# Kernel tuning notes

Measured on AMD Instinct MI355X. Metric: run time of the kernel, lower is better.

Reference implementation:

```python
import jax, jax.numpy as jnp
from jax import lax
import numpy as np

KS, STRIDE, RATE, SCALE = 3, 1, 2, 10.0  # module init kwargs


def _resize_bilinear_ac(x, oh, ow):
    # F.interpolate(mode='bilinear', align_corners=True); x: [B,C,H,W]
    H, W = x.shape[2], x.shape[3]
    ys = jnp.linspace(0.0, H - 1.0, oh)
    xs = jnp.linspace(0.0, W - 1.0, ow)
    y0 = jnp.floor(ys).astype(jnp.int32)
    y1 = jnp.minimum(y0 + 1, H - 1)
    wy = (ys - y0)[:, None]
    x0 = jnp.floor(xs).astype(jnp.int32)
    x1 = jnp.minimum(x0 + 1, W - 1)
    wx = xs - x0
    g = lambda yi, xi: x[:, :, yi, :][:, :, :, xi]
    top = g(y0, x0) * (1 - wx) + g(y0, x1) * wx
    bot = g(y1, x0) * (1 - wx) + g(y1, x1) * wx
    return top * (1 - wy) + bot * wy


def _conv3x3(x, w, b):
    y = lax.conv_general_dilated(x, w, (1, 1), ((1, 1), (1, 1)),
                                 dimension_numbers=('NCHW', 'OIHW', 'NCHW'))
    return y + b[None, :, None, None]


def _extract_patches(x, k, s):
    # mirrors extract_patches(): ZeroPad2d(1) when k != 1, then unfold h,w
    if k != 1:
        x = jnp.pad(x, ((0, 0), (0, 0), (1, 1), (1, 1)))
    b, c, h, w = x.shape
    nh = (h - k) // s + 1
    nw = (w - k) // s + 1
    cols = jnp.stack([x[:, :, i:i + s * (nh - 1) + 1:s, j:j + s * (nw - 1) + 1:s]
                      for i in range(k) for j in range(k)], axis=-1)  # [B,C,nh,nw,k*k]
    return cols.reshape(b, c, nh, nw, k, k).transpose(0, 2, 3, 1, 4, 5).reshape(b, nh * nw, c, k, k)


def _instance_norm(x, eps=1e-5):
    mu = x.mean((2, 3), keepdims=True)
    var = ((x - mu) ** 2).mean((2, 3), keepdims=True)
    return (x - mu) * lax.rsqrt(var + eps)


def _conv_transpose(att, w):
    # torch F.conv_transpose2d(att, w, stride=2, padding=1); att [Q,h,w], w [Q,Cout,4,4]
    rhs = jnp.flip(w, (-2, -1)).transpose(1, 0, 2, 3)  # [Cout,Q,4,4]
    return lax.conv_general_dilated(att[None], rhs, (1, 1), ((2, 2), (2, 2)),
                                    lhs_dilation=(2, 2),
                                    dimension_numbers=('NCHW', 'OIHW', 'NCHW'))[0]


def _forward(background, foreground, mask, Wc, bc, Wm, bm, Wf, bf):
    h, w = foreground.shape[2], foreground.shape[3]
    mask64 = _resize_bilinear_ac(mask, h, w)
    fg_c = foreground * (1 - mask64)
    fg_m = foreground * mask64
    bg_c = background * (1 - mask64)
    bg_m = background * mask64
    # ODConv2d(fg, bg) stand-in: plain 3x3 conv on the fused features
    bg_c = _conv3x3(fg_c + bg_c, Wc, bc)
    bg_m = _conv3x3(fg_m + bg_m, Wm, bm)
    x = _conv3x3(bg_c + bg_m, Wf, bf)
    x = _instance_norm(x)
    x = x * jax.nn.sigmoid(x)  # MemoryEfficientSwish
    b = x.shape[0]
    raw_w = _extract_patches(x, 2 * RATE, STRIDE * RATE)       # [B,1024,256,4,4]
    x_down = _resize_bilinear_ac(x, h // RATE, w // RATE)       # [B,256,32,32]
    hd, wd = x_down.shape[2], x_down.shape[3]
    pt = _extract_patches(x_down, KS, STRIDE)                   # [B,1024,256,3,3]
    mask32 = _resize_bilinear_ac(mask64, hd, wd)
    mpt = _extract_patches(mask32, KS, STRIDE)                  # [B,1024,1,3,3]
    mm = (mpt.mean((2, 3, 4)) == 0.0).astype(x.dtype)[:, :, None, None]  # [B,1024,1,1]
    norm = jnp.sqrt((pt * pt).sum((2, 3, 4), keepdims=True))
    w_normed = pt / jnp.maximum(norm, 1e-4)
    # score = F.conv2d(x_down, w_normed, padding=1): batched patch-attention GEMM
    score = jnp.einsum('bqckl,bpckl->bqp', w_normed, pt).reshape(b, hd * wd, hd, wd)
    score = score * mm
    att = jax.nn.softmax(score * SCALE, axis=1) * mm
    att = jnp.clip(att, 1e-8, None)
    f1 = jax.vmap(_conv_transpose)(att, raw_w) / 4.0            # [B,256,64,64]
    return f1 * mask64 + x * (1 - mask64)


def setup_inputs() -> dict:
    key = jax.random.key(0)
    ks = jax.random.split(key, 9)
    B, C, H, W = 8, 256, 64, 64
    background = jax.random.normal(ks[0], (B, C, H, W), jnp.float32)
    foreground = jax.random.normal(ks[1], (B, C, H, W), jnp.float32)
    # blocky binary hole mask (16x16 blocks upsampled to 256x256)
    m0 = (jax.random.uniform(ks[2], (B, 1, 16, 16)) > 0.5).astype(jnp.float32)
    mask = jnp.repeat(jnp.repeat(m0, 16, axis=2), 16, axis=3)
    s = 0.05
    Wc = jax.random.normal(ks[3], (256, 256, 3, 3), jnp.float32) * s
    bc = jax.random.normal(ks[4], (256,), jnp.float32) * s
    Wm = jax.random.normal(ks[5], (256, 256, 3, 3), jnp.float32) * s
    bm = jax.random.normal(ks[6], (256,), jnp.float32) * s
    Wf = jax.random.normal(ks[7], (256, 256, 3, 3), jnp.float32) * s
    bf = jax.random.normal(ks[8], (256,), jnp.float32) * s
    return {'background': background, 'foreground': foreground, 'mask': mask,
            'Wc': Wc, 'bc': bc, 'Wm': Wm, 'bm': bm, 'Wf': Wf, 'bf': bf}


def reference(background, foreground, mask, Wc, bc, Wm, bm, Wf, bf):
    return _forward(background, foreground, mask, Wc, bc, Wm, bm, Wf, bf)
```

## Files before the change

kernel.cpp:

```cpp
#include <hip/hip_runtime.h>
#include <math.h>

#define B_ 8
#define C_ 256
#define NPIX 4096
#define NP 1024

typedef __attribute__((ext_vector_type(8))) short bf16x8;
typedef __attribute__((ext_vector_type(4))) float f32x4;

#define GLL16(src, dst) __builtin_amdgcn_global_load_lds( \
    (__attribute__((address_space(1))) void*)(src), \
    (__attribute__((address_space(3))) void*)(dst), 16, 0, 0)

__device__ __forceinline__ unsigned short f2bf(float f) {
  unsigned int u = __float_as_uint(f);
  unsigned int r = (u + 0x7FFFu + ((u >> 16) & 1u)) >> 16;
  return (unsigned short)r;
}
__device__ __forceinline__ unsigned int pk2(unsigned short lo, unsigned short hi) {
  return (unsigned int)lo | ((unsigned int)hi << 16);
}

__device__ __forceinline__ float wave_reduce_sum(float v) {
#pragma unroll
  for (int off = 32; off > 0; off >>= 1) v += __shfl_down(v, off, 64);
  return v;
}
__device__ __forceinline__ float wave_reduce_max(float v) {
#pragma unroll
  for (int off = 32; off > 0; off >>= 1) v = fmaxf(v, __shfl_down(v, off, 64));
  return v;
}

__global__ __launch_bounds__(256) void k_resize(const float* __restrict__ in, float* __restrict__ out,
                                                int IH, int IW, int OH, int OW, int nElem) {
  int idx = blockIdx.x * 256 + threadIdx.x;
  if (idx >= nElem) return;
  int ox = idx % OW; int t = idx / OW; int oy = t % OH; int bc = t / OH;
  float dy = (float)(IH - 1) / (float)(OH - 1);
  float dx = (float)(IW - 1) / (float)(OW - 1);
  float yf = (float)oy * dy;
  float xf = (float)ox * dx;
  float y0f = floorf(yf), x0f = floorf(xf);
  int y0 = (int)y0f, x0 = (int)x0f;
  int y1 = min(y0 + 1, IH - 1), x1 = min(x0 + 1, IW - 1);
  float wy = yf - y0f, wx = xf - x0f;
  const float* p = in + (size_t)bc * IH * IW;
  float a = p[y0 * IW + x0], b = p[y0 * IW + x1];
  float c = p[y1 * IW + x0], d = p[y1 * IW + x1];
  float top = a * (1.0f - wx) + b * wx;
  float bot = c * (1.0f - wx) + d * wx;
  out[idx] = top * (1.0f - wy) + bot * wy;
}

__global__ __launch_bounds__(256) void k_wprep(const float* __restrict__ Wc, const float* __restrict__ Wm,
                                               const float* __restrict__ Wf,
                                               unsigned short* __restrict__ Wp1, unsigned short* __restrict__ Wp2) {
  int idx = blockIdx.x * 256 + threadIdx.x;
  if (idx >= 3 * 589824) return;
  int part = idx / 589824;
  int rem = idx % 589824;
  int kk = rem >> 16, co = (rem >> 8) & 255, ci = rem & 255;
  const float* W = (part == 0) ? Wc : (part == 1) ? Wm : Wf;
  unsigned short o = f2bf(W[(size_t)co * 2304 + ci * 9 + kk]);
  if (part == 0) Wp1[rem] = o;
  else if (part == 1) Wp1[589824 + rem] = o;
  else Wp2[rem] = o;
}

__global__ __launch_bounds__(256) void k_bias(const float* __restrict__ bc, const float* __restrict__ bm,
                                              float* __restrict__ bias1, float* __restrict__ zpg) {
  int i = threadIdx.x;
  bias1[i] = bc[i] + bm[i];
  for (int j = i; j < 2048; j += 256) zpg[j] = 0.f;
}

__global__ __launch_bounds__(256) void k_prepAT(const float* __restrict__ fg, const float* __restrict__ bg,
                                                const float* __restrict__ m64,
                                                unsigned short* __restrict__ A0t, unsigned short* __restrict__ A1t) {
  __shared__ unsigned short T0[64][66];
  __shared__ unsigned short T1[64][66];
  int pt = blockIdx.x, ct = blockIdx.y, b = blockIdx.z;
  int pix0 = pt << 6, ci0 = ct << 6;
  int tid = threadIdx.x;
  {
    int r = tid >> 2, c4 = (tid & 3) << 4;
    size_t ib = (((size_t)(b * 256 + ci0 + r)) << 12) + pix0 + c4;
    const float* fb = fg + ib;
    const float* gb = bg + ib;
    const float* mb = m64 + (((size_t)b) << 12) + pix0 + c4;
#pragma unroll
    for (int k = 0; k < 16; k += 4) {
      float4 f = *(const float4*)(fb + k);
      float4 g = *(const float4*)(gb + k);
      float4 m = *(const float4*)(mb + k);
      float s0 = f.x + g.x, s1 = f.y + g.y, s2 = f.z + g.z, s3 = f.w + g.w;
      T0[r][c4 + k + 0] = f2bf(s0 * (1.f - m.x));
      T0[r][c4 + k + 1] = f2bf(s1 * (1.f - m.y));
      T0[r][c4 + k + 2] = f2bf(s2 * (1.f - m.z));
      T0[r][c4 + k + 3] = f2bf(s3 * (1.f - m.w));
      T1[r][c4 + k + 0] = f2bf(s0 * m.x);
      T1[r][c4 + k + 1] = f2bf(s1 * m.y);
      T1[r][c4 + k + 2] = f2bf(s2 * m.z);
      T1[r][c4 + k + 3] = f2bf(s3 * m.w);
    }
  }
  __syncthreads();
  {
    int pr = tid >> 2, cc = (tid & 3) << 4;
    unsigned int o0[8], o1[8];
#pragma unroll
    for (int k = 0; k < 8; k++) {
      o0[k] = pk2(T0[cc + 2 * k][pr], T0[cc + 2 * k + 1][pr]);
      o1[k] = pk2(T1[cc + 2 * k][pr], T1[cc + 2 * k + 1][pr]);
    }
    size_t ob = ((((size_t)b << 12) + pix0 + pr) << 8) + ci0 + cc;
    *(uint4*)&A0t[ob] = *(uint4*)&o0[0];
    *(uint4*)&A0t[ob + 8] = *(uint4*)&o0[4];
    *(uint4*)&A1t[ob] = *(uint4*)&o1[0];
    *(uint4*)&A1t[ob + 8] = *(uint4*)&o1[4];
  }
}

__device__ __forceinline__ int swz(int row, int slot) {
  return row * 32 + ((slot ^ (row & 3) ^ ((row >> 2) & 3)) << 3);
}

template <int NKK, bool OUT_TRANS_BF16>
__global__ __launch_bounds__(256, 2) void k_conv2ph(const unsigned short* __restrict__ A0t,
                                                    const unsigned short* __restrict__ A1t,
                                                    const unsigned short* __restrict__ Wp,
                                                    const float* __restrict__ bias,
                                                    const unsigned short* __restrict__ zp,
                                                    void* __restrict__ outp) {
  __shared__ __align__(16) unsigned short AB[2][8192];
  int wgl = blockIdx.x + 32 * (blockIdx.y + 2 * blockIdx.z);
  int nid = (wgl & 7) * 64 + (wgl >> 3);
  int bp = nid & 31, cot = (nid >> 5) & 1, b = nid >> 6;
  int tid = threadIdx.x, lane = tid & 63, w3 = tid >> 6;
  int wm = w3 >> 1, wn = w3 & 1;

  int rA = w3 * 32 + (lane >> 2), rA1 = rA + 16;
  int ds0 = (lane & 3) ^ (rA & 3) ^ ((rA >> 2) & 3);
  int ds1 = (lane & 3) ^ (rA1 & 3) ^ ((rA1 >> 2) & 3);
  int y_0 = bp * 2 + (rA >> 6), x_0 = rA & 63;
  int y_1 = bp * 2 + (rA1 >> 6), x_1 = rA1 & 63;
  int co_0 = cot * 128 + rA, co_1 = cot * 128 + rA1;

  f32x4 acc[4][4];
#pragma unroll
  for (int i = 0; i < 4; i++)
#pragma unroll
    for (int j = 0; j < 4; j++) acc[i][j] = (f32x4){0.f, 0.f, 0.f, 0.f};

  const unsigned short *pA0, *pA1, *pB0, *pB1;

#define UPDATE(kkv) {                                                           \
    int kk_ = (kkv);                                                            \
    int kw_ = (NKK == 18 && kk_ >= 9) ? kk_ - 9 : kk_;                          \
    const unsigned short* Asrc_ = (NKK == 18 && kk_ >= 9) ? A1t : A0t;          \
    int ky_ = kw_ / 3 - 1, kx_ = kw_ % 3 - 1;                                   \
    int yy0_ = y_0 + ky_, xx0_ = x_0 + kx_;                                     \
    int yy1_ = y_1 + ky_, xx1_ = x_1 + kx_;                                     \
    pA0 = ((unsigned)yy0_ < 64u && (unsigned)xx0_ < 64u)                        \
        ? Asrc_ + ((((size_t)(b << 6) + yy0_) << 6) + xx0_) * 256 + ds0 * 8     \
        : zp + ds0 * 8;                                                         \
    pA1 = ((unsigned)yy1_ < 64u && (unsigned)xx1_ < 64u)                        \
        ? Asrc_ + ((((size_t)(b << 6) + yy1_) << 6) + xx1_) * 256 + ds1 * 8     \
        : zp + ds1 * 8;                                                         \
    pB0 = Wp + ((size_t)kk_ << 16) + co_0 * 256 + ds0 * 8;                      \
    pB1 = Wp + ((size_t)kk_ << 16) + co_1 * 256 + ds1 * 8;                      \
  }
#define STAGE(c2, buf) {                                                        \
    int ci0_ = ((c2) & 7) << 5;                                                 \
    unsigned short* lb_ = &AB[buf][0];                                          \
    GLL16(pA0 + ci0_, lb_ + w3 * 1024);                                         \
    GLL16(pA1 + ci0_, lb_ + w3 * 1024 + 512);                                   \
    GLL16(pB0 + ci0_, lb_ + 4096 + w3 * 1024);                                  \
    GLL16(pB1 + ci0_, lb_ + 4096 + w3 * 1024 + 512);                            \
  }

  const int NCH = NKK * 8;
  UPDATE(0);
  STAGE(0, 0);
  for (int c = 0; c < NCH; ++c) {
    asm volatile("" ::: "memory");
    __builtin_amdgcn_s_barrier();
    asm volatile("" ::: "memory");
    if (c < NCH - 1) {
      int cn = c + 1;
      if ((cn & 7) == 0) UPDATE(cn >> 3);
      STAGE(cn, cn & 1);
      asm volatile("s_waitcnt vmcnt(4)" ::: "memory");
    } else {
      asm volatile("s_waitcnt vmcnt(0)" ::: "memory");
    }
    __builtin_amdgcn_s_barrier();
    asm volatile("" ::: "memory");
    const unsigned short* Al = &AB[c & 1][0];
    const unsigned short* Bl = &AB[c & 1][4096];
    int slot = lane >> 4;
    int mr = wm * 64 + (lane & 15), ncc = wn * 64 + (lane & 15);
    bf16x8 af[4], bfr[4];
#pragma unroll
    for (int i = 0; i < 4; i++) af[i] = *(const bf16x8*)&Al[swz(mr + i * 16, slot)];
#pragma unroll
    for (int j = 0; j < 4; j++) bfr[j] = *(const bf16x8*)&Bl[swz(ncc + j * 16, slot)];
#pragma unroll
    for (int i = 0; i < 4; i++)
#pragma unroll
      for (int j = 0; j < 4; j++)
        acc[i][j] = __builtin_amdgcn_mfma_f32_16x16x32_bf16(af[i], bfr[j], acc[i][j], 0, 0, 0);
  }
#undef STAGE
#undef UPDATE

  int px0 = bp * 128 + wm * 64 + ((lane >> 4) << 2);
  int co0 = cot * 128 + wn * 64 + (lane & 15);
#pragma unroll
  for (int j = 0; j < 4; j++) {
    int co = co0 + j * 16;
    float bs = bias[co];
#pragma unroll
    for (int i = 0; i < 4; i++) {
#pragma unroll
      for (int r = 0; r < 4; r++) {
        float v = acc[i][j][r] + bs;
        int pix = px0 + i * 16 + r;
        if (OUT_TRANS_BF16)
          ((unsigned short*)outp)[((((size_t)b << 12) + pix) << 8) + co] = f2bf(v);
        else
          ((float*)outp)[((((size_t)b << 8) + co) << 12) + pix] = v;
      }
    }
  }
}

__global__ __launch_bounds__(256) void k_innorm(float* __restrict__ x) {
  __shared__ float s4[4];
  int bc = blockIdx.x;
  float* p = x + (size_t)bc * NPIX;
  int tid = threadIdx.x;
  int lane = tid & 63, w = tid >> 6;
  float v[16];
  float s = 0.f;
#pragma unroll
  for (int i = 0; i < 16; i++) { v[i] = p[tid + i * 256]; s += v[i]; }
  s = wave_reduce_sum(s);
  if (lane == 0) s4[w] = s;
  __syncthreads();
  float mean = (s4[0] + s4[1] + s4[2] + s4[3]) * (1.0f / 4096.0f);
  __syncthreads();
  float s2 = 0.f;
#pragma unroll
  for (int i = 0; i < 16; i++) { float d = v[i] - mean; s2 += d * d; }
  s2 = wave_reduce_sum(s2);
  if (lane == 0) s4[w] = s2;
  __syncthreads();
  float var = (s4[0] + s4[1] + s4[2] + s4[3]) * (1.0f / 4096.0f);
  float inv = 1.0f / sqrtf(var + 1e-5f);
#pragma unroll
  for (int i = 0; i < 16; i++) {
    float xn = (v[i] - mean) * inv;
    float sg = 1.0f / (1.0f + expf(-xn));
    p[tid + i * 256] = xn * sg;
  }
}

__global__ __launch_bounds__(256) void k_trans_xd(const float* __restrict__ xd,
                                                  unsigned short* __restrict__ xdt) {
  __shared__ unsigned short T[64][66];
  int qt = blockIdx.x, ct = blockIdx.y, b = blockIdx.z;
  int q0 = qt << 6, ci0 = ct << 6;
  int tid = threadIdx.x;
  {
    int r = tid >> 2, c4 = (tid & 3) << 4;
    const float* xb = xd + (((size_t)(b * 256 + ci0 + r)) << 10) + q0 + c4;
#pragma unroll
    for (int k = 0; k < 16; k += 4) {
      float4 f = *(const float4*)(xb + k);
      T[r][c4 + k + 0] = f2bf(f.x);
      T[r][c4 + k + 1] = f2bf(f.y);
      T[r][c4 + k + 2] = f2bf(f.z);
      T[r][c4 + k + 3] = f2bf(f.w);
    }
  }
  __syncthreads();
  {
    int qr = tid >> 2, cc = (tid & 3) << 4;
    unsigned int o[8];
#pragma unroll
    for (int k = 0; k < 8; k++) o[k] = pk2(T[cc + 2 * k][qr], T[cc + 2 * k + 1][qr]);
    size_t ob = ((((size_t)b << 10) + q0 + qr) << 8) + ci0 + cc;
    *(uint4*)&xdt[ob] = *(uint4*)&o[0];
    *(uint4*)&xdt[ob + 8] = *(uint4*)&o[4];
  }
}

__global__ __launch_bounds__(256) void k_sq32(const float* __restrict__ xd, float* __restrict__ sq) {
  int idx = blockIdx.x * 256 + threadIdx.x;
  if (idx >= B_ * NP) return;
  int pix = idx & 1023; int b = idx >> 10;
  const float* p = xd + (size_t)b * C_ * NP + pix;
  float s = 0.f;
  for (int c = 0; c < C_; c++) { float v = p[c * NP]; s += v * v; }
  sq[idx] = s;
}

__global__ __launch_bounds__(256) void k_normmm(const float* __restrict__ sq, const float* __restrict__ m32,
                                                float* __restrict__ fq) {
  int idx = blockIdx.x * 256 + threadIdx.x;
  if (idx >= B_ * NP) return;
  int q = idx & 1023, b = idx >> 10;
  int qi = q >> 5, qj = q & 31;
  float ns = 0.f, ms = 0.f;
#pragma unroll
  for (int k = 0; k < 3; k++)
#pragma unroll
    for (int l = 0; l < 3; l++) {
      int r = qi + k - 1, c = qj + l - 1;
      if (r >= 0 && r < 32 && c >= 0 && c < 32) {
        ns += sq[b * NP + r * 32 + c];
        ms += m32[b * NP + r * 32 + c];
      }
    }
  float f = (ms == 0.0f) ? (1.0f / fmaxf(sqrtf(ns), 1e-4f)) : 0.0f;
  fq[idx] = f;
}

__global__ __launch_bounds__(256, 2) void k_gram2ph(const unsigned short* __restrict__ xdt,
                                                    const float* __restrict__ fq,
                                                    const unsigned short* __restrict__ zp,
                                                    float* __restrict__ sc) {
  __shared__ __align__(16) unsigned short AB[2][8192];
  int wgl = blockIdx.x + 8 * (blockIdx.y + 8 * blockIdx.z);
  int nid = (wgl & 7) * 64 + (wgl >> 3);
  int bp = nid & 7, bq = (nid >> 3) & 7, b = nid >> 6;
  int tid = threadIdx.x, lane = tid & 63, w3 = tid >> 6;
  int wm = w3 >> 1, wn = w3 & 1;

  int rA = w3 * 32 + (lane >> 2), rA1 = rA + 16;
  int ds0 = (lane & 3) ^ (rA & 3) ^ ((rA >> 2) & 3);
  int ds1 = (lane & 3) ^ (rA1 & 3) ^ ((rA1 >> 2) & 3);
  int pA0r = bp * 128 + rA, pA1r = bp * 128 + rA1;
  int pB0r = bq * 128 + rA, pB1r = bq * 128 + rA1;
  int piA0 = pA0r >> 5, pjA0 = pA0r & 31, piA1 = pA1r >> 5, pjA1 = pA1r & 31;
  int piB0 = pB0r >> 5, pjB0 = pB0r & 31, piB1 = pB1r >> 5, pjB1 = pB1r & 31;
  const unsigned short* xb = xdt + (((size_t)b) << 18);

  f32x4 acc[4][4];
#pragma unroll
  for (int i = 0; i < 4; i++)
#pragma unroll
    for (int j = 0; j < 4; j++) acc[i][j] = (f32x4){0.f, 0.f, 0.f, 0.f};

  const unsigned short *pA0, *pA1, *pB0, *pB1;

#define GUPDATE(kkv) {                                                          \
    int kk_ = (kkv);                                                            \
    int dy_ = kk_ / 3 - 1, dx_ = kk_ % 3 - 1;                                   \
    int ya0 = piA0 + dy_, xa0 = pjA0 + dx_;                                     \
    int ya1 = piA1 + dy_, xa1 = pjA1 + dx_;                                     \
    int yb0 = piB0 + dy_, xb0 = pjB0 + dx_;                                     \
    int yb1 = piB1 + dy_, xb1 = pjB1 + dx_;                                     \
    pA0 = ((unsigned)ya0 < 32u && (unsigned)xa0 < 32u)                          \
        ? xb + ((((size_t)ya0 << 5) + xa0) << 8) + ds0 * 8 : zp + ds0 * 8;      \
    pA1 = ((unsigned)ya1 < 32u && (unsigned)xa1 < 32u)                          \
        ? xb + ((((size_t)ya1 << 5) + xa1) << 8) + ds1 * 8 : zp + ds1 * 8;      \
    pB0 = ((unsigned)yb0 < 32u && (unsigned)xb0 < 32u)                          \
        ? xb + ((((size_t)yb0 << 5) + xb0) << 8) + ds0 * 8 : zp + ds0 * 8;      \
    pB1 = ((unsigned)yb1 < 32u && (unsigned)xb1 < 32u)                          \
        ? xb + ((((size_t)yb1 << 5) + xb1) << 8) + ds1 * 8 : zp + ds1 * 8;      \
  }
#define GSTAGE(c2, buf) {                                                       \
    int ci0_ = ((c2) & 7) << 5;                                                 \
    unsigned short* lb_ = &AB[buf][0];                                          \
    GLL16(pA0 + ci0_, lb_ + w3 * 1024);                                         \
    GLL16(pA1 + ci0_, lb_ + w3 * 1024 + 512);                                   \
    GLL16(pB0 + ci0_, lb_ + 4096 + w3 * 1024);                                  \
    GLL16(pB1 + ci0_, lb_ + 4096 + w3 * 1024 + 512);                            \
  }

  GUPDATE(0);
  GSTAGE(0, 0);
  for (int c = 0; c < 72; ++c) {
    asm volatile("" ::: "memory");
    __builtin_amdgcn_s_barrier();
    asm volatile("" ::: "memory");
    if (c < 71) {
      int cn = c + 1;
      if ((cn & 7) == 0) GUPDATE(cn >> 3);
      GSTAGE(cn, cn & 1);
      asm volatile("s_waitcnt vmcnt(4)" ::: "memory");
    } else {
      asm volatile("s_waitcnt vmcnt(0)" ::: "memory");
    }
    __builtin_amdgcn_s_barrier();
    asm volatile("" ::: "memory");
    const unsigned short* Al = &AB[c & 1][0];
    const unsigned short* Bl = &AB[c & 1][4096];
    int slot = lane >> 4;
    int mr = wm * 64 + (lane & 15), ncc = wn * 64 + (lane & 15);
    bf16x8 af[4], bfr[4];
#pragma unroll
    for (int i = 0; i < 4; i++) af[i] = *(const bf16x8*)&Al[swz(mr + i * 16, slot)];
#pragma unroll
    for (int j = 0; j < 4; j++) bfr[j] = *(const bf16x8*)&Bl[swz(ncc + j * 16, slot)];
#pragma unroll
    for (int i = 0; i < 4; i++)
#pragma unroll
      for (int j = 0; j < 4; j++)
        acc[i][j] = __builtin_amdgcn_mfma_f32_16x16x32_bf16(af[i], bfr[j], acc[i][j], 0, 0, 0);
  }
#undef GSTAGE
#undef GUPDATE

  int q0 = bq * 128 + wn * 64 + (lane & 15);
  int p0 = bp * 128 + wm * 64 + ((lane >> 4) << 2);
#pragma unroll
  for (int j = 0; j < 4; j++) {
    int q = q0 + j * 16;
    float f = fq[(b << 10) + q];
#pragma unroll
    for (int i = 0; i < 4; i++)
#pragma unroll
      for (int r = 0; r < 4; r++)
        sc[((size_t)(b << 10) + (p0 + i * 16 + r)) * NP + q] = acc[i][j][r] * f;
  }
}

__global__ __launch_bounds__(256) void k_softmax(const float* __restrict__ sc, const float* __restrict__ fq,
                                                 unsigned short* __restrict__ attb) {
  __shared__ float s4[4];
  int row = blockIdx.x;
  int b = row >> 10;
  const float* r = sc + (size_t)row * NP;
  int tid = threadIdx.x;
  int lane = tid & 63, w = tid >> 6;
  float4 sv = *(const float4*)&r[tid * 4];
  float l0 = sv.x * 10.f, l1 = sv.y * 10.f, l2 = sv.z * 10.f, l3 = sv.w * 10.f;
  float mx = fmaxf(fmaxf(l0, l1), fmaxf(l2, l3));
  mx = wave_reduce_max(mx);
  if (lane == 0) s4[w] = mx;
  __syncthreads();
  float M = fmaxf(fmaxf(s4[0], s4[1]), fmaxf(s4[2], s4[3]));
  __syncthreads();
  float e0 = expf(l0 - M), e1 = expf(l1 - M), e2 = expf(l2 - M), e3 = expf(l3 - M);
  float s = e0 + e1 + e2 + e3;
  s = wave_reduce_sum(s);
  if (lane == 0) s4[w] = s;
  __syncthreads();
  float inv = 1.0f / (s4[0] + s4[1] + s4[2] + s4[3]);
  const float* fb = fq + b * NP + tid * 4;
  float m0 = fb[0] > 0.f ? 1.f : 0.f;
  float m1 = fb[1] > 0.f ? 1.f : 0.f;
  float m2 = fb[2] > 0.f ? 1.f : 0.f;
  float m3 = fb[3] > 0.f ? 1.f : 0.f;
  float a0 = fmaxf(e0 * inv * m0, 1e-8f);
  float a1 = fmaxf(e1 * inv * m1, 1e-8f);
  float a2 = fmaxf(e2 * inv * m2, 1e-8f);
  float a3 = fmaxf(e3 * inv * m3, 1e-8f);
  uint2 o;
  o.x = pk2(f2bf(a0), f2bf(a1));
  o.y = pk2(f2bf(a2), f2bf(a3));
  *(uint2*)&attb[(size_t)row * NP + tid * 4] = o;
}

__global__ __launch_bounds__(256) void k_xprep(const float* __restrict__ x,
                                               unsigned short* __restrict__ P0,
                                               unsigned short* __restrict__ P1,
                                               unsigned short* __restrict__ P2) {
  int idx = blockIdx.x * 256 + threadIdx.x;
  int xh8 = idx & 3;
  int yh = (idx >> 2) & 31;
  int co = (idx >> 7) & 255;
  int pc = (idx >> 15) & 3;
  int b  = idx >> 17;
  int cy = pc >> 1, cx = pc & 1;
  const float* row = x + ((size_t)(b * 256 + co) * 64 + (2 * yh + cy)) * 64 + 16 * xh8;
  float4 f0 = *(const float4*)(row);
  float4 f1 = *(const float4*)(row + 4);
  float4 f2 = *(const float4*)(row + 8);
  float4 f3 = *(const float4*)(row + 12);
  unsigned short v0 = f2bf(cx ? f0.y : f0.x), v1 = f2bf(cx ? f0.w : f0.z);
  unsigned short v2 = f2bf(cx ? f1.y : f1.x), v3 = f2bf(cx ? f1.w : f1.z);
  unsigned short v4 = f2bf(cx ? f2.y : f2.x), v5 = f2bf(cx ? f2.w : f2.z);
  unsigned short v6 = f2bf(cx ? f3.y : f3.x), v7 = f2bf(cx ? f3.w : f3.z);
  int prev = __shfl_up((int)v7, 1, 64);
  int next = __shfl_down((int)v0, 1, 64);
  unsigned short pv = (xh8 == 0) ? (unsigned short)0 : (unsigned short)prev;
  unsigned short nx = (xh8 == 3) ? (unsigned short)0 : (unsigned short)next;
  size_t base = ((size_t)((b * 4 + pc) * 256 + co) * 32 + yh) * 32 + 8 * xh8;
  uint4 w0 = {pk2(v0, v1), pk2(v2, v3), pk2(v4, v5), pk2(v6, v7)};
  *(uint4*)&P0[base] = w0;
  uint4 w1 = {pk2(pv, v0), pk2(v1, v2), pk2(v3, v4), pk2(v5, v6)};
  *(uint4*)&P1[base] = w1;
  uint4 w2 = {pk2(v1, v2), pk2(v3, v4), pk2(v5, v6), pk2(v7, nx)};
  *(uint4*)&P2[base] = w2;
}

__global__ __launch_bounds__(256, 2) void k_pv(const unsigned short* __restrict__ attb,
                                               const unsigned short* __restrict__ P0,
                                               const unsigned short* __restrict__ P1,
                                               const unsigned short* __restrict__ P2,
                                               const unsigned short* __restrict__ zp,
                                               const float* __restrict__ xbuf,
                                               const float* __restrict__ m64,
                                               float* __restrict__ out) {
  __shared__ __align__(16) unsigned short AB[2][8192];
  int wg = blockIdx.x + blockIdx.y * 8 + blockIdx.z * 16;
  int nid = (wg & 7) * 64 + (wg >> 3);
  int bn = nid & 7, bm = (nid >> 3) & 1, z = nid >> 4;
  int b = z >> 2, cls = z & 3, cy = cls >> 1, cx = cls & 1;
  int tid = threadIdx.x, lane = tid & 63, w3 = tid >> 6;
  int wm = w3 >> 1, wn = w3 & 1;

  int dy1 = cy ? -1 : 1;
  int pio1 = cy ? 1 : -1;
  int pjo1 = cx ? 1 : -1;
  const unsigned short* Pdx = cx ? P1 : P2;

  int rA0 = w3 * 32 + (lane >> 2);
  int rA1 = rA0 + 16;
  int ds0 = (lane & 3) ^ (rA0 & 3) ^ ((rA0 >> 2) & 3);
  int ds1 = (lane & 3) ^ (rA1 & 3) ^ ((rA1 >> 2) & 3);
  int offA0 = ((z * 256 + bm * 128 + rA0) << 10) + ds0 * 8;
  int offA1 = ((z * 256 + bm * 128 + rA1) << 10) + ds1 * 8;

  const unsigned short* attB = attb + ((size_t)b << 20);
  int o0 = bn * 128 + rA0, o1 = bn * 128 + rA1;
  int oy0 = o0 >> 5, ox0 = o0 & 31, oy1 = o1 >> 5, ox1 = o1 & 31;
#define BPTR(oyv, oxv, dsv, tyv, txv) ({                                        \
    int pi = (oyv) + ((tyv) ? pio1 : 0);                                        \
    int pj = (oxv) + ((txv) ? pjo1 : 0);                                        \
    (pi >= 0 && pi < 32 && pj >= 0 && pj < 32)                                  \
        ? attB + (((pi << 5) + pj) << 10) + (dsv) * 8 : zp; })
  const unsigned short* b0t0 = BPTR(oy0, ox0, ds0, 0, 0);
  const unsigned short* b0t1 = BPTR(oy0, ox0, ds0, 0, 1);
  const unsigned short* b0t2 = BPTR(oy0, ox0, ds0, 1, 0);
  const unsigned short* b0t3 = BPTR(oy0, ox0, ds0, 1, 1);
  const unsigned short* b1t0 = BPTR(oy1, ox1, ds1, 0, 0);
  const unsigned short* b1t1 = BPTR(oy1, ox1, ds1, 0, 1);
  const unsigned short* b1t2 = BPTR(oy1, ox1, ds1, 1, 0);
  const unsigned short* b1t3 = BPTR(oy1, ox1, ds1, 1, 1);
#undef BPTR

  f32x4 acc[4][4];
#pragma unroll
  for (int i = 0; i < 4; i++)
#pragma unroll
    for (int j = 0; j < 4; j++) acc[i][j] = (f32x4){0.f, 0.f, 0.f, 0.f};

  int dA0 = w3 * 1024, dA1 = w3 * 1024 + 512;
  int dB0 = 4096 + w3 * 1024, dB1 = 4096 + w3 * 1024 + 512;

#define PSTAGE(c2, buf) {                                                       \
    int t2 = (c2) >> 5, qi = (c2) & 31;                                         \
    int q32 = qi * 32;                                                          \
    const unsigned short* Ab = (t2 & 1) ? Pdx : P0;                             \
    int dyo = (t2 >> 1) ? dy1 * 32 : 0;                                         \
    bool vA = (t2 < 2) || ((dy1 > 0) ? (qi < 31) : (qi > 0));                   \
    if (!vA) Ab = zp;                                                           \
    int oA0 = vA ? offA0 + dyo + q32 : 0;                                       \
    int oA1 = vA ? offA1 + dyo + q32 : 0;                                       \
    unsigned short* lb = &AB[buf][0];                                           \
    GLL16(Ab + oA0, lb + dA0);                                                  \
    GLL16(Ab + oA1, lb + dA1);                                                  \
    const unsigned short* sB0 = (t2 == 0 ? b0t0 : t2 == 1 ? b0t1 : t2 == 2 ? b0t2 : b0t3) + q32; \
    const unsigned short* sB1 = (t2 == 0 ? b1t0 : t2 == 1 ? b1t1 : t2 == 2 ? b1t2 : b1t3) + q32; \
    GLL16(sB0, lb + dB0);                                                       \
    GLL16(sB1, lb + dB1);                                                       \
  }

  PSTAGE(0, 0);
  for (int c = 0; c < 128; ++c) {
    asm volatile("" ::: "memory");
    __builtin_amdgcn_s_barrier();
    asm volatile("" ::: "memory");
    if (c < 127) {
      PSTAGE(c + 1, (c + 1) & 1);
      asm volatile("s_waitcnt vmcnt(4)" ::: "memory");
    } else {
      asm volatile("s_waitcnt vmcnt(0)" ::: "memory");
    }
    __builtin_amdgcn_s_barrier();
    asm volatile("" ::: "memory");
    const unsigned short* Al = &AB[c & 1][0];
    const unsigned short* Bl = &AB[c & 1][4096];
    int slot = lane >> 4;
    int mr = wm * 64 + (lane & 15), ncc = wn * 64 + (lane & 15);
    bf16x8 af[4], bfr[4];
#pragma unroll
    for (int i = 0; i < 4; i++) af[i] = *(const bf16x8*)&Al[swz(mr + i * 16, slot)];
#pragma unroll
    for (int j = 0; j < 4; j++) bfr[j] = *(const bf16x8*)&Bl[swz(ncc + j * 16, slot)];
#pragma unroll
    for (int i = 0; i < 4; i++)
#pragma unroll
      for (int j = 0; j < 4; j++)
        acc[i][j] = __builtin_amdgcn_mfma_f32_16x16x32_bf16(af[i], bfr[j], acc[i][j], 0, 0, 0);
  }
#undef PSTAGE

  int co0 = bm * 128 + wm * 64 + ((lane >> 4) << 2);
  int oo0 = bn * 128 + wn * 64 + (lane & 15);
#pragma unroll
  for (int j = 0; j < 4; j++) {
    int o = oo0 + j * 16;
    int oy = ((o >> 5) << 1) + cy, ox = ((o & 31) << 1) + cx;
    int opix = oy * 64 + ox;
    float msk = m64[b * NPIX + opix];
    float s = 0.25f * msk, t1m = 1.0f - msk;
#pragma unroll
    for (int i = 0; i < 4; i++) {
#pragma unroll
      for (int r = 0; r < 4; r++) {
        int co = co0 + i * 16 + r;
        size_t xi = (size_t)(b * C_ + co) * NPIX + opix;
        out[xi] = acc[i][j][r] * s + xbuf[xi] * t1m;
      }
    }
  }
}

extern "C" void kernel_launch(void* const* d_in, const int* in_sizes, int n_in,
                              void* d_out, int out_size, void* d_ws, size_t ws_size,
                              hipStream_t stream) {
  const float* bg   = (const float*)d_in[0];
  const float* fg   = (const float*)d_in[1];
  const float* mask = (const float*)d_in[2];
  const float* Wc   = (const float*)d_in[3];
  const float* bc   = (const float*)d_in[4];
  const float* Wm   = (const float*)d_in[5];
  const float* bm   = (const float*)d_in[6];
  const float* Wf   = (const float*)d_in[7];
  const float* bf   = (const float*)d_in[8];
  float* out = (float*)d_out;
  float* w = (float*)d_ws;

  float* mask64 = w;
  float* mask32 = w + 32768;
  float* sq32   = w + 40960;
  float* fq     = w + 49152;
  float* bias1  = w + 57344;
  float* zpage  = w + 57600;
  unsigned short* A0t = (unsigned short*)(w + 65536);
  unsigned short* A1t = (unsigned short*)(w + 65536 + 4194304);
  float* sc = w + 65536;
  unsigned short* P0u = (unsigned short*)(w + 65536);
  unsigned short* P1u = (unsigned short*)(w + 4259840);
  unsigned short* tbuf_t = (unsigned short*)(w + 8454144);
  float* xd = w + 8454144;
  unsigned short* xdt = (unsigned short*)(w + 10551296);
  unsigned short* attb = (unsigned short*)(w + 8454144);
  float* xbuf = w + 12648448;
  unsigned short* Wp1 = (unsigned short*)(w + 21037056);
  unsigned short* Wp2 = (unsigned short*)(w + 21626880);
  unsigned short* P2u = (unsigned short*)(w + 21037056);

  const unsigned short* zp = (const unsigned short*)zpage;

  hipLaunchKernelGGL(k_resize, dim3(128), dim3(256), 0, stream, mask, mask64, 256, 256, 64, 64, 32768);
  hipLaunchKernelGGL(k_wprep, dim3(6912), dim3(256), 0, stream, Wc, Wm, Wf, Wp1, Wp2);
  hipLaunchKernelGGL(k_bias, dim3(1), dim3(256), 0, stream, bc, bm, bias1, zpage);
  hipLaunchKernelGGL(k_prepAT, dim3(64, 4, 8), dim3(256), 0, stream, fg, bg, mask64, A0t, A1t);
  hipLaunchKernelGGL((k_conv2ph<18, true>), dim3(32, 2, 8), dim3(256), 0, stream,
                     A0t, A1t, Wp1, bias1, zp, (void*)tbuf_t);
  hipLaunchKernelGGL((k_conv2ph<9, false>), dim3(32, 2, 8), dim3(256), 0, stream,
                     tbuf_t, tbuf_t, Wp2, bf, zp, (void*)xbuf);
  hipLaunchKernelGGL(k_innorm, dim3(B_ * C_), dim3(256), 0, stream, xbuf);
  hipLaunchKernelGGL(k_resize, dim3(8192), dim3(256), 0, stream, xbuf, xd, 64, 64, 32, 32, B_ * C_ * NP);
  hipLaunchKernelGGL(k_resize, dim3(32), dim3(256), 0, stream, mask64, mask32, 64, 64, 32, 32, B_ * NP);
  hipLaunchKernelGGL(k_trans_xd, dim3(16, 4, 8), dim3(256), 0, stream, xd, xdt);
  hipLaunchKernelGGL(k_sq32, dim3(32), dim3(256), 0, stream, xd, sq32);
  hipLaunchKernelGGL(k_normmm, dim3(32), dim3(256), 0, stream, sq32, mask32, fq);
  hipLaunchKernelGGL(k_gram2ph, dim3(8, 8, 8), dim3(256), 0, stream, xdt, fq, zp, sc);
  hipLaunchKernelGGL(k_softmax, dim3(B_ * NP), dim3(256), 0, stream, sc, fq, attb);
  hipLaunchKernelGGL(k_xprep, dim3(4096), dim3(256), 0, stream, xbuf, P0u, P1u, P2u);
  hipLaunchKernelGGL(k_pv, dim3(8, 2, 32), dim3(256), 0, stream, attb, P0u, P1u, P2u,
                     zp, xbuf, mask64, out);
}
```

Baseline: 356.1 us.

## Double K-chunk per barrier in MFMA GEMMs and fuse norm with downsample

```diff
diff --git a/kernel.cpp b/kernel.cpp
--- a/kernel.cpp
+++ b/kernel.cpp
@@ -134,7 +134,7 @@
                                                     const float* __restrict__ bias,
                                                     const unsigned short* __restrict__ zp,
                                                     void* __restrict__ outp) {
-  __shared__ __align__(16) unsigned short AB[2][8192];
+  __shared__ __align__(16) unsigned short AB[2][16384];
   int wgl = blockIdx.x + 32 * (blockIdx.y + 2 * blockIdx.z);
   int nid = (wgl & 7) * 64 + (wgl >> 3);
   int bp = nid & 31, cot = (nid >> 5) & 1, b = nid >> 6;
@@ -173,15 +173,19 @@
     pB1 = Wp + ((size_t)kk_ << 16) + co_1 * 256 + ds1 * 8;                      \
   }
 #define STAGE(c2, buf) {                                                        \
-    int ci0_ = ((c2) & 7) << 5;                                                 \
+    int ci0_ = ((c2) & 3) << 6;                                                 \
     unsigned short* lb_ = &AB[buf][0];                                          \
-    GLL16(pA0 + ci0_, lb_ + w3 * 1024);                                         \
-    GLL16(pA1 + ci0_, lb_ + w3 * 1024 + 512);                                   \
-    GLL16(pB0 + ci0_, lb_ + 4096 + w3 * 1024);                                  \
-    GLL16(pB1 + ci0_, lb_ + 4096 + w3 * 1024 + 512);                            \
-  }
-
-  const int NCH = NKK * 8;
+    GLL16(pA0 + ci0_,      lb_ + w3 * 1024);                                    \
+    GLL16(pA1 + ci0_,      lb_ + w3 * 1024 + 512);                              \
+    GLL16(pA0 + ci0_ + 32, lb_ + 4096 + w3 * 1024);                             \
+    GLL16(pA1 + ci0_ + 32, lb_ + 4096 + w3 * 1024 + 512);                       \
+    GLL16(pB0 + ci0_,      lb_ + 8192 + w3 * 1024);                             \
+    GLL16(pB1 + ci0_,      lb_ + 8192 + w3 * 1024 + 512);                       \
+    GLL16(pB0 + ci0_ + 32, lb_ + 12288 + w3 * 1024);                            \
+    GLL16(pB1 + ci0_ + 32, lb_ + 12288 + w3 * 1024 + 512);                      \
+  }
+
+  const int NCH = NKK * 4;
   UPDATE(0);
   STAGE(0, 0);
   for (int c = 0; c < NCH; ++c) {
@@ -190,28 +194,31 @@
     asm volatile("" ::: "memory");
     if (c < NCH - 1) {
       int cn = c + 1;
-      if ((cn & 7) == 0) UPDATE(cn >> 3);
+      if ((cn & 3) == 0) UPDATE(cn >> 2);
       STAGE(cn, cn & 1);
-      asm volatile("s_waitcnt vmcnt(4)" ::: "memory");
+      asm volatile("s_waitcnt vmcnt(8)" ::: "memory");
     } else {
       asm volatile("s_waitcnt vmcnt(0)" ::: "memory");
     }
     __builtin_amdgcn_s_barrier();
     asm volatile("" ::: "memory");
-    const unsigned short* Al = &AB[c & 1][0];
-    const unsigned short* Bl = &AB[c & 1][4096];
     int slot = lane >> 4;
     int mr = wm * 64 + (lane & 15), ncc = wn * 64 + (lane & 15);
-    bf16x8 af[4], bfr[4];
-#pragma unroll
-    for (int i = 0; i < 4; i++) af[i] = *(const bf16x8*)&Al[swz(mr + i * 16, slot)];
-#pragma unroll
-    for (int j = 0; j < 4; j++) bfr[j] = *(const bf16x8*)&Bl[swz(ncc + j * 16, slot)];
-#pragma unroll
-    for (int i = 0; i < 4; i++)
-#pragma unroll
-      for (int j = 0; j < 4; j++)
-        acc[i][j] = __builtin_amdgcn_mfma_f32_16x16x32_bf16(af[i], bfr[j], acc[i][j], 0, 0, 0);
+#pragma unroll
+    for (int ks = 0; ks < 2; ++ks) {
+      const unsigned short* Al = &AB[c & 1][ks << 12];
+      const unsigned short* Bl = &AB[c & 1][8192 + (ks << 12)];
+      bf16x8 af[4], bfr[4];
+#pragma unroll
+      for (int i = 0; i < 4; i++) af[i] = *(const bf16x8*)&Al[swz(mr + i * 16, slot)];
+#pragma unroll
+      for (int j = 0; j < 4; j++) bfr[j] = *(const bf16x8*)&Bl[swz(ncc + j * 16, slot)];
+#pragma unroll
+      for (int i = 0; i < 4; i++)
+#pragma unroll
+        for (int j = 0; j < 4; j++)
+          acc[i][j] = __builtin_amdgcn_mfma_f32_16x16x32_bf16(af[i], bfr[j], acc[i][j], 0, 0, 0);
+    }
   }
 #undef STAGE
 #undef UPDATE
@@ -237,7 +244,8 @@
   }
 }
 
-__global__ __launch_bounds__(256) void k_innorm(float* __restrict__ x) {
+__global__ __launch_bounds__(256) void k_post(float* __restrict__ x, float* __restrict__ xd) {
+  __shared__ float sL[4096];
   __shared__ float s4[4];
   int bc = blockIdx.x;
   float* p = x + (size_t)bc * NPIX;
@@ -264,7 +272,28 @@
   for (int i = 0; i < 16; i++) {
     float xn = (v[i] - mean) * inv;
     float sg = 1.0f / (1.0f + expf(-xn));
-    p[tid + i * 256] = xn * sg;
+    float o = xn * sg;
+    p[tid + i * 256] = o;
+    sL[tid + i * 256] = o;
+  }
+  __syncthreads();
+  float dyx = 63.0f / 31.0f;
+  float* xdp = xd + (size_t)bc * NP;
+#pragma unroll
+  for (int k = 0; k < 4; k++) {
+    int q = tid + k * 256;
+    int yq = q >> 5, xq = q & 31;
+    float yf = (float)yq * dyx;
+    float xf = (float)xq * dyx;
+    float y0f = floorf(yf), x0f = floorf(xf);
+    int y0 = (int)y0f, x0 = (int)x0f;
+    int y1 = min(y0 + 1, 63), x1 = min(x0 + 1, 63);
+    float wy = yf - y0f, wx = xf - x0f;
+    float a = sL[y0 * 64 + x0], b2 = sL[y0 * 64 + x1];
+    float c2 = sL[y1 * 64 + x0], d2 = sL[y1 * 64 + x1];
+    float top = a * (1.0f - wx) + b2 * wx;
+    float bot = c2 * (1.0f - wx) + d2 * wx;
+    xdp[q] = top * (1.0f - wy) + bot * wy;
   }
 }
 
@@ -308,12 +337,14 @@
   sq[idx] = s;
 }
 
-__global__ __launch_bounds__(256) void k_normmm(const float* __restrict__ sq, const float* __restrict__ m32,
-                                                float* __restrict__ fq) {
+__global__ __launch_bounds__(256) void k_fq(const float* __restrict__ sq, const float* __restrict__ m64,
+                                            float* __restrict__ fq) {
   int idx = blockIdx.x * 256 + threadIdx.x;
   if (idx >= B_ * NP) return;
   int q = idx & 1023, b = idx >> 10;
   int qi = q >> 5, qj = q & 31;
+  const float* mb = m64 + (b << 12);
+  float dyx = 63.0f / 31.0f;
   float ns = 0.f, ms = 0.f;
 #pragma unroll
   for (int k = 0; k < 3; k++)
@@ -322,7 +353,16 @@
       int r = qi + k - 1, c = qj + l - 1;
       if (r >= 0 && r < 32 && c >= 0 && c < 32) {
         ns += sq[b * NP + r * 32 + c];
-        ms += m32[b * NP + r * 32 + c];
+        float yf = (float)r * dyx, xf = (float)c * dyx;
+        float y0f = floorf(yf), x0f = floorf(xf);
+        int y0 = (int)y0f, x0 = (int)x0f;
+        int y1 = min(y0 + 1, 63), x1 = min(x0 + 1, 63);
+        float wy = yf - y0f, wx = xf - x0f;
+        float a = mb[y0 * 64 + x0], b2 = mb[y0 * 64 + x1];
+        float c2 = mb[y1 * 64 + x0], d2 = mb[y1 * 64 + x1];
+        float top = a * (1.0f - wx) + b2 * wx;
+        float bot = c2 * (1.0f - wx) + d2 * wx;
+        ms += top * (1.0f - wy) + bot * wy;
       }
     }
   float f = (ms == 0.0f) ? (1.0f / fmaxf(sqrtf(ns), 1e-4f)) : 0.0f;
@@ -333,7 +373,7 @@
                                                     const float* __restrict__ fq,
                                                     const unsigned short* __restrict__ zp,
                                                     float* __restrict__ sc) {
-  __shared__ __align__(16) unsigned short AB[2][8192];
+  __shared__ __align__(16) unsigned short AB[2][16384];
   int wgl = blockIdx.x + 8 * (blockIdx.y + 8 * blockIdx.z);
   int nid = (wgl & 7) * 64 + (wgl >> 3);
   int bp = nid & 7, bq = (nid >> 3) & 7, b = nid >> 6;
@@ -374,44 +414,51 @@
         ? xb + ((((size_t)yb1 << 5) + xb1) << 8) + ds1 * 8 : zp + ds1 * 8;      \
   }
 #define GSTAGE(c2, buf) {                                                       \
-    int ci0_ = ((c2) & 7) << 5;                                                 \
+    int ci0_ = ((c2) & 3) << 6;                                                 \
     unsigned short* lb_ = &AB[buf][0];                                          \
-    GLL16(pA0 + ci0_, lb_ + w3 * 1024);                                         \
-    GLL16(pA1 + ci0_, lb_ + w3 * 1024 + 512);                                   \
-    GLL16(pB0 + ci0_, lb_ + 4096 + w3 * 1024);                                  \
-    GLL16(pB1 + ci0_, lb_ + 4096 + w3 * 1024 + 512);                            \
+    GLL16(pA0 + ci0_,      lb_ + w3 * 1024);                                    \
+    GLL16(pA1 + ci0_,      lb_ + w3 * 1024 + 512);                              \
+    GLL16(pA0 + ci0_ + 32, lb_ + 4096 + w3 * 1024);                             \
+    GLL16(pA1 + ci0_ + 32, lb_ + 4096 + w3 * 1024 + 512);                       \
+    GLL16(pB0 + ci0_,      lb_ + 8192 + w3 * 1024);                             \
+    GLL16(pB1 + ci0_,      lb_ + 8192 + w3 * 1024 + 512);                       \
+    GLL16(pB0 + ci0_ + 32, lb_ + 12288 + w3 * 1024);                            \
+    GLL16(pB1 + ci0_ + 32, lb_ + 12288 + w3 * 1024 + 512);                      \
   }
 
   GUPDATE(0);
   GSTAGE(0, 0);
-  for (int c = 0; c < 72; ++c) {
+  for (int c = 0; c < 36; ++c) {
     asm volatile("" ::: "memory");
     __builtin_amdgcn_s_barrier();
     asm volatile("" ::: "memory");
-    if (c < 71) {
+    if (c < 35) {
       int cn = c + 1;
-      if ((cn & 7) == 0) GUPDATE(cn >> 3);
+      if ((cn & 3) == 0) GUPDATE(cn >> 2);
       GSTAGE(cn, cn & 1);
-      asm volatile("s_waitcnt vmcnt(4)" ::: "memory");
+      asm volatile("s_waitcnt vmcnt(8)" ::: "memory");
     } else {
       asm volatile("s_waitcnt vmcnt(0)" ::: "memory");
     }
     __builtin_amdgcn_s_barrier();
     asm volatile("" ::: "memory");
-    const unsigned short* Al = &AB[c & 1][0];
-    const unsigned short* Bl = &AB[c & 1][4096];
     int slot = lane >> 4;
     int mr = wm * 64 + (lane & 15), ncc = wn * 64 + (lane & 15);
-    bf16x8 af[4], bfr[4];
-#pragma unroll
-    for (int i = 0; i < 4; i++) af[i] = *(const bf16x8*)&Al[swz(mr + i * 16, slot)];
-#pragma unroll
-    for (int j = 0; j < 4; j++) bfr[j] = *(const bf16x8*)&Bl[swz(ncc + j * 16, slot)];
-#pragma unroll
-    for (int i = 0; i < 4; i++)
-#pragma unroll
-      for (int j = 0; j < 4; j++)
-        acc[i][j] = __builtin_amdgcn_mfma_f32_16x16x32_bf16(af[i], bfr[j], acc[i][j], 0, 0, 0);
+#pragma unroll
+    for (int ks = 0; ks < 2; ++ks) {
+      const unsigned short* Al = &AB[c & 1][ks << 12];
+      const unsigned short* Bl = &AB[c & 1][8192 + (ks << 12)];
+      bf16x8 af[4], bfr[4];
+#pragma unroll
+      for (int i = 0; i < 4; i++) af[i] = *(const bf16x8*)&Al[swz(mr + i * 16, slot)];
+#pragma unroll
+      for (int j = 0; j < 4; j++) bfr[j] = *(const bf16x8*)&Bl[swz(ncc + j * 16, slot)];
+#pragma unroll
+      for (int i = 0; i < 4; i++)
+#pragma unroll
+        for (int j = 0; j < 4; j++)
+          acc[i][j] = __builtin_amdgcn_mfma_f32_16x16x32_bf16(af[i], bfr[j], acc[i][j], 0, 0, 0);
+    }
   }
 #undef GSTAGE
 #undef GUPDATE
@@ -508,7 +555,7 @@
                                                const float* __restrict__ xbuf,
                                                const float* __restrict__ m64,
                                                float* __restrict__ out) {
-  __shared__ __align__(16) unsigned short AB[2][8192];
+  __shared__ __align__(16) unsigned short AB[2][16384];
   int wg = blockIdx.x + blockIdx.y * 8 + blockIdx.z * 16;
   int nid = (wg & 7) * 64 + (wg >> 3);
   int bn = nid & 7, bm = (nid >> 3) & 1, z = nid >> 4;
@@ -553,10 +600,10 @@
     for (int j = 0; j < 4; j++) acc[i][j] = (f32x4){0.f, 0.f, 0.f, 0.f};
 
   int dA0 = w3 * 1024, dA1 = w3 * 1024 + 512;
-  int dB0 = 4096 + w3 * 1024, dB1 = 4096 + w3 * 1024 + 512;
-
-#define PSTAGE(c2, buf) {                                                       \
-    int t2 = (c2) >> 5, qi = (c2) & 31;                                         \
+  int dB0 = 8192 + w3 * 1024, dB1 = 8192 + w3 * 1024 + 512;
+
+#define PHALF(o2, buf, h) {                                                     \
+    int t2 = (o2) >> 5, qi = (o2) & 31;                                         \
     int q32 = qi * 32;                                                          \
     const unsigned short* Ab = (t2 & 1) ? Pdx : P0;                             \
     int dyo = (t2 >> 1) ? dy1 * 32 : 0;                                         \
@@ -564,7 +611,7 @@
     if (!vA) Ab = zp;                                                           \
     int oA0 = vA ? offA0 + dyo + q32 : 0;                                       \
     int oA1 = vA ? offA1 + dyo + q32 : 0;                                       \
-    unsigned short* lb = &AB[buf][0];                                           \
+    unsigned short* lb = &AB[buf][(h) << 12];                                   \
     GLL16(Ab + oA0, lb + dA0);                                                  \
     GLL16(Ab + oA1, lb + dA1);                                                  \
     const unsigned short* sB0 = (t2 == 0 ? b0t0 : t2 == 1 ? b0t1 : t2 == 2 ? b0t2 : b0t3) + q32; \
@@ -572,36 +619,41 @@
     GLL16(sB0, lb + dB0);                                                       \
     GLL16(sB1, lb + dB1);                                                       \
   }
+#define PSTAGE(c2, buf) { PHALF(2 * (c2), buf, 0); PHALF(2 * (c2) + 1, buf, 1); }
 
   PSTAGE(0, 0);
-  for (int c = 0; c < 128; ++c) {
+  for (int c = 0; c < 64; ++c) {
     asm volatile("" ::: "memory");
     __builtin_amdgcn_s_barrier();
     asm volatile("" ::: "memory");
-    if (c < 127) {
+    if (c < 63) {
       PSTAGE(c + 1, (c + 1) & 1);
-      asm volatile("s_waitcnt vmcnt(4)" ::: "memory");
+      asm volatile("s_waitcnt vmcnt(8)" ::: "memory");
     } else {
       asm volatile("s_waitcnt vmcnt(0)" ::: "memory");
     }
     __builtin_amdgcn_s_barrier();
     asm volatile("" ::: "memory");
-    const unsigned short* Al = &AB[c & 1][0];
-    const unsigned short* Bl = &AB[c & 1][4096];
     int slot = lane >> 4;
     int mr = wm * 64 + (lane & 15), ncc = wn * 64 + (lane & 15);
-    bf16x8 af[4], bfr[4];
-#pragma unroll
-    for (int i = 0; i < 4; i++) af[i] = *(const bf16x8*)&Al[swz(mr + i * 16, slot)];
-#pragma unroll
-    for (int j = 0; j < 4; j++) bfr[j] = *(const bf16x8*)&Bl[swz(ncc + j * 16, slot)];
-#pragma unroll
-    for (int i = 0; i < 4; i++)
-#pragma unroll
-      for (int j = 0; j < 4; j++)
-        acc[i][j] = __builtin_amdgcn_mfma_f32_16x16x32_bf16(af[i], bfr[j], acc[i][j], 0, 0, 0);
+#pragma unroll
+    for (int ks = 0; ks < 2; ++ks) {
+      const unsigned short* Al = &AB[c & 1][ks << 12];
+      const unsigned short* Bl = &AB[c & 1][8192 + (ks << 12)];
+      bf16x8 af[4], bfr[4];
+#pragma unroll
+      for (int i = 0; i < 4; i++) af[i] = *(const bf16x8*)&Al[swz(mr + i * 16, slot)];
+#pragma unroll
+      for (int j = 0; j < 4; j++) bfr[j] = *(const bf16x8*)&Bl[swz(ncc + j * 16, slot)];
+#pragma unroll
+      for (int i = 0; i < 4; i++)
+#pragma unroll
+        for (int j = 0; j < 4; j++)
+          acc[i][j] = __builtin_amdgcn_mfma_f32_16x16x32_bf16(af[i], bfr[j], acc[i][j], 0, 0, 0);
+    }
   }
 #undef PSTAGE
+#undef PHALF
 
   int co0 = bm * 128 + wm * 64 + ((lane >> 4) << 2);
   int oo0 = bn * 128 + wn * 64 + (lane & 15);
@@ -640,7 +692,6 @@
   float* w = (float*)d_ws;
 
   float* mask64 = w;
-  float* mask32 = w + 32768;
   float* sq32   = w + 40960;
   float* fq     = w + 49152;
   float* bias1  = w + 57344;
@@ -669,12 +720,10 @@
                      A0t, A1t, Wp1, bias1, zp, (void*)tbuf_t);
   hipLaunchKernelGGL((k_conv2ph<9, false>), dim3(32, 2, 8), dim3(256), 0, stream,
                      tbuf_t, tbuf_t, Wp2, bf, zp, (void*)xbuf);
-  hipLaunchKernelGGL(k_innorm, dim3(B_ * C_), dim3(256), 0, stream, xbuf);
-  hipLaunchKernelGGL(k_resize, dim3(8192), dim3(256), 0, stream, xbuf, xd, 64, 64, 32, 32, B_ * C_ * NP);
-  hipLaunchKernelGGL(k_resize, dim3(32), dim3(256), 0, stream, mask64, mask32, 64, 64, 32, 32, B_ * NP);
+  hipLaunchKernelGGL(k_post, dim3(B_ * C_), dim3(256), 0, stream, xbuf, xd);
   hipLaunchKernelGGL(k_trans_xd, dim3(16, 4, 8), dim3(256), 0, stream, xd, xdt);
   hipLaunchKernelGGL(k_sq32, dim3(32), dim3(256), 0, stream, xd, sq32);
-  hipLaunchKernelGGL(k_normmm, dim3(32), dim3(256), 0, stream, sq32, mask32, fq);
+  hipLaunchKernelGGL(k_fq, dim3(32), dim3(256), 0, stream, sq32, mask64, fq);
   hipLaunchKernelGGL(k_gram2ph, dim3(8, 8, 8), dim3(256), 0, stream, xdt, fq, zp, sc);
   hipLaunchKernelGGL(k_softmax, dim3(B_ * NP), dim3(256), 0, stream, sc, fq, attb);
   hipLaunchKernelGGL(k_xprep, dim3(4096), dim3(256), 0, stream, xbuf, P0u, P1u, P2u);
```

New measurement: 338.3 us. 1.05x faster.
